# Kernel tuning notes

Hardware: AMD Instinct MI355X
Metric: run time of the kernel (lower is better)

## Reference

```python
import jax, jax.numpy as jnp
import numpy as np

B, S, D, H, DC, HC, M = 2, 2048, 1024, 16, 64, 16, 4096
DH = D // H  # head_dim = 64


def _ln(x, g, b, eps=1e-5):
    m = jnp.mean(x, axis=-1, keepdims=True)
    v = jnp.var(x, axis=-1, keepdims=True)
    return (x - m) * jax.lax.rsqrt(v + eps) * g + b


def setup_inputs() -> dict:
    key = jax.random.key(0)
    ks = jax.random.split(key, 10)
    def w(k, shape, fan_in):
        return jax.random.normal(k, shape, jnp.float32) * (fan_in ** -0.5)
    return {
        "h": jax.random.normal(ks[0], (B, S, D), jnp.float32),
        "z": jax.random.normal(ks[1], (B, S, DC), jnp.float32),
        # Linear weights stored [in, out] (transpose of torch layout)
        "wv": w(ks[2], (D, D), D),   "bv": jnp.zeros((D,), jnp.float32),
        "wca": w(ks[3], (DC, H * HC), DC), "bca": jnp.zeros((H * HC,), jnp.float32),
        "wcn": w(ks[4], (D, DC), D), "bcn": jnp.zeros((DC,), jnp.float32),
        "wo": w(ks[5], (D, D), D),   "bo": jnp.zeros((D,), jnp.float32),
        "gamma": jnp.zeros((1, H, 1, 1), jnp.float32),
        "w1": w(ks[6], (D, M), D),   "b1": jnp.zeros((M,), jnp.float32),
        "w2": w(ks[7], (M, D), M),   "b2": jnp.zeros((D,), jnp.float32),
        "ln1_g": jnp.ones((D,), jnp.float32),  "ln1_b": jnp.zeros((D,), jnp.float32),
        "ln2_g": jnp.ones((D,), jnp.float32),  "ln2_b": jnp.zeros((D,), jnp.float32),
        "lnc_g": jnp.ones((DC,), jnp.float32), "lnc_b": jnp.zeros((DC,), jnp.float32),
    }


def reference(h, z, wv, bv, wca, bca, wcn, bcn, wo, bo, gamma,
              w1, b1, w2, b2, ln1_g, ln1_b, ln2_g, ln2_b, lnc_g, lnc_b):
    hn = _ln(h, ln1_g, ln1_b)
    # values: [B,S,H,DH]
    value = (hn @ wv + bv).reshape(B, S, H, DH)
    # per-head coordinates: [B,S,H,HC]
    zh = (z @ wca + bca).reshape(B, S, H, HC)
    # pairwise squared distances per head: ||zq||^2 + ||zk||^2 - 2 zq.zk
    z_sq = jnp.sum(zh * zh, axis=-1).transpose(0, 2, 1)        # [B,H,S]
    dot = jnp.einsum('bqhc,bkhc->bhqk', zh, zh)                # [B,H,S,S]
    sq_dist = jnp.maximum(z_sq[:, :, :, None] + z_sq[:, :, None, :] - 2.0 * dot, 0.0)
    g = jax.nn.softplus(gamma)                                 # [1,H,1,1]
    attn = jax.nn.softmax(-g * sq_dist, axis=-1)               # [B,H,S,S]
    attn_out = jnp.einsum('bhqk,bkhd->bqhd', attn, value).reshape(B, S, D)
    h_attn = attn_out @ wo + bo
    z_next = hn @ wcn + bcn
    h = h + h_attn
    # FFN (dropout is identity in eval); torch GELU default is exact (erf)
    hn2 = _ln(h, ln2_g, ln2_b)
    ffn = jax.nn.gelu(hn2 @ w1 + b1, approximate=False) @ w2 + b2
    h = h + ffn
    z_out = _ln(z + z_next, lnc_g, lnc_b)
    return h, z_out
```

## Files before the change

### kernel.cpp

```cpp
#include <hip/hip_runtime.h>

#define USH unsigned short

__device__ __forceinline__ float b2f(USH u) {
    union { unsigned int i; float f; } x; x.i = ((unsigned int)u) << 16; return x.f;
}
__device__ __forceinline__ USH f2b(float f) {
    union { float f; unsigned int i; } x; x.f = f;
    unsigned int r = x.i + (0x7fffu + ((x.i >> 16) & 1u));
    return (USH)(r >> 16);
}
__device__ __forceinline__ float ldf(const USH* p)  { return b2f(*p); }
__device__ __forceinline__ float ldf(const float* p){ return *p; }
__device__ __forceinline__ void stf(USH* p, float v)  { *p = f2b(v); }
__device__ __forceinline__ void stf(float* p, float v){ *p = v; }

#define GLOAD16(gp, lp) __builtin_amdgcn_global_load_lds(                     \
    (const __attribute__((address_space(1))) void*)(gp),                      \
    (__attribute__((address_space(3))) void*)(lp), 16, 0, 0)

typedef __attribute__((ext_vector_type(8))) __bf16 bf16x8;
typedef __attribute__((ext_vector_type(4))) float  floatx4;

__global__ __launch_bounds__(256) void transpose_f2b(const float* __restrict__ W,
                                                     USH* __restrict__ WT,
                                                     int K, int N) {
    __shared__ USH t[64][72];
    int n0 = blockIdx.x * 64, k0 = blockIdx.y * 64;
    int tid = threadIdx.x;
    int kr = tid >> 4, nc = (tid & 15) * 4;
#pragma unroll
    for (int r = 0; r < 4; r++) {
        int k = kr + r * 16;
        float4 v = *(const float4*)(W + (size_t)(k0 + k) * N + n0 + nc);
        t[nc + 0][k] = f2b(v.x); t[nc + 1][k] = f2b(v.y);
        t[nc + 2][k] = f2b(v.z); t[nc + 3][k] = f2b(v.w);
    }
    __syncthreads();
    int nr = tid >> 2, kc = (tid & 3) * 8;
#pragma unroll
    for (int r = 0; r < 2; r++) {
        int k = kc + r * 32;
        *(int4*)(WT + (size_t)(n0 + nr) * K + k0 + k) = *(const int4*)&t[nr][k];
    }
}

template <typename TX>
__global__ __launch_bounds__(256) void ln_rows(const TX* __restrict__ x,
                                               const float* __restrict__ g,
                                               const float* __restrict__ bb,
                                               USH* __restrict__ y) {
    int row = blockIdx.x, tid = threadIdx.x;
    const TX* xr = x + (size_t)row * 1024 + tid * 4;
    float v[4];
#pragma unroll
    for (int i = 0; i < 4; i++) v[i] = ldf(xr + i);
    float s  = v[0] + v[1] + v[2] + v[3];
    float ss = v[0]*v[0] + v[1]*v[1] + v[2]*v[2] + v[3]*v[3];
#pragma unroll
    for (int o = 32; o; o >>= 1) { s += __shfl_down(s, o); ss += __shfl_down(ss, o); }
    __shared__ float red[10];
    int w = tid >> 6;
    if ((tid & 63) == 0) { red[w] = s; red[4 + w] = ss; }
    __syncthreads();
    if (tid == 0) {
        float S = red[0] + red[1] + red[2] + red[3];
        float SS = red[4] + red[5] + red[6] + red[7];
        float mean = S * (1.f / 1024.f);
        float var  = SS * (1.f / 1024.f) - mean * mean;
        red[8] = mean; red[9] = rsqrtf(var + 1e-5f);
    }
    __syncthreads();
    float mean = red[8], rstd = red[9];
    USH* yr = y + (size_t)row * 1024 + tid * 4;
#pragma unroll
    for (int i = 0; i < 4; i++) {
        int c = tid * 4 + i;
        yr[i] = f2b((v[i] - mean) * rstd * g[c] + bb[c]);
    }
}

__global__ __launch_bounds__(256) void zh_kernel(const float* __restrict__ z,
                                                 const float* __restrict__ wca,
                                                 const float* __restrict__ bca,
                                                 const float* __restrict__ gamma,
                                                 USH* __restrict__ zq_pack,
                                                 USH* __restrict__ zk_pack) {
    int row = blockIdx.x, n = threadIdx.x;
    __shared__ float zrow[64];
    if (n < 64) zrow[n] = z[(size_t)row * 64 + n];
    __syncthreads();
    float s = bca[n];
#pragma unroll 8
    for (int k = 0; k < 64; k++) s = fmaf(zrow[k], wca[(size_t)k * 256 + n], s);
    int h = n >> 4, c = n & 15;
    float gvl = log1pf(__expf(gamma[h])) * 1.44269504f;
    USH u = f2b(s);
    float sv = b2f(u);
    float sq = sv * sv;
    sq += __shfl_xor(sq, 1); sq += __shfl_xor(sq, 2);
    sq += __shfl_xor(sq, 4); sq += __shfl_xor(sq, 8);
    size_t base = ((size_t)h * 4096 + row) * 32;
    zk_pack[base + c] = u;
    zq_pack[base + c] = f2b(2.f * gvl * s);
    if (c == 0) {
        USH hi = f2b(sq);
        float lo = sq - b2f(hi);
        unsigned int kw0 = 0x3F80u | ((unsigned int)hi << 16);
        unsigned int kw1 = (unsigned int)f2b(lo);
        uint4 kv = {kw0, kw1, 0u, 0u};
        uint4 zz = {0u, 0u, 0u, 0u};
        *(uint4*)(zk_pack + base + 16) = kv;
        *(uint4*)(zk_pack + base + 24) = zz;
        unsigned int qw0 = (unsigned int)f2b(-gvl * sq) | ((unsigned int)f2b(-gvl) << 16);
        unsigned int qw1 = (unsigned int)f2b(-gvl);
        uint4 qv = {qw0, qw1, 0u, 0u};
        *(uint4*)(zq_pack + base + 16) = qv;
        *(uint4*)(zq_pack + base + 24) = zz;
    }
}

template <int EPI, int MI, int NI, int KB, typename TRES, typename TOUT>
__global__ __launch_bounds__(256) void gemm_kernel(const USH* __restrict__ A,
                                                   const USH* __restrict__ WT,
                                                   const float* __restrict__ bias,
                                                   const TRES* __restrict__ res,
                                                   TOUT* __restrict__ out,
                                                   int M, int N, int K) {
    constexpr int BM  = MI * 32;
    constexpr int BN  = NI * 32;
    constexpr int GR  = KB / 8;
    constexpr int RPC = 2048 / KB;
    constexpr int ACH = BM / RPC;
    constexpr int BCH = BN / RPC;
    __shared__ __align__(16) USH lA[BM][KB];
    __shared__ __align__(16) USH lB[BN][KB];
    int tid = threadIdx.x;
    int lane = tid & 63, wave = tid >> 6;
    int wr = wave >> 1, wc = wave & 1;
    int quad = lane >> 4, l15 = lane & 15;
    int m0 = blockIdx.x * BM, n0 = blockIdx.y * BN;

    int srow = tid / GR;
    int kg   = tid % GR;
    int scol = (kg ^ (srow & 7)) * 8;

    const USH* gA = A + (size_t)(m0 + srow) * K + scol;
    const USH* gB = WT + (size_t)(n0 + srow) * K + scol;
    USH* lA0 = &lA[0][0] + tid * 8;
    USH* lB0 = &lB[0][0] + tid * 8;
    int xo = (l15 & 7) * 8;

    floatx4 acc[MI][NI] = {};

    for (int k0 = 0; k0 < K; k0 += KB) {
#pragma unroll
        for (int c = 0; c < ACH; c++)
            GLOAD16(gA + (size_t)c * RPC * K + k0, lA0 + c * 2048);
#pragma unroll
        for (int c = 0; c < BCH; c++)
            GLOAD16(gB + (size_t)c * RPC * K + k0, lB0 + c * 2048);
        __syncthreads();

#pragma unroll
        for (int ks = 0; ks < KB / 32; ks++) {
            bf16x8 bfr[NI];
#pragma unroll
            for (int ni = 0; ni < NI; ni++)
                bfr[ni] = *(const bf16x8*)&lB[wc * (NI * 16) + ni * 16 + l15][(ks * 32 + quad * 8) ^ xo];
#pragma unroll
            for (int mi = 0; mi < MI; mi++) {
                bf16x8 afr = *(const bf16x8*)&lA[wr * (MI * 16) + mi * 16 + l15][(ks * 32 + quad * 8) ^ xo];
#pragma unroll
                for (int ni = 0; ni < NI; ni++)
                    acc[mi][ni] = __builtin_amdgcn_mfma_f32_16x16x32_bf16(afr, bfr[ni], acc[mi][ni], 0, 0, 0);
            }
        }
        __syncthreads();
    }

    float bias_v[NI];
#pragma unroll
    for (int ni = 0; ni < NI; ni++) bias_v[ni] = bias[n0 + wc * (NI * 16) + ni * 16 + l15];

#pragma unroll
    for (int mi = 0; mi < MI; mi++) {
#pragma unroll
        for (int r = 0; r < 4; r++) {
            int row = m0 + wr * (MI * 16) + mi * 16 + quad * 4 + r;
            size_t base = (size_t)row * N;
#pragma unroll
            for (int ni = 0; ni < NI; ni++) {
                int col = n0 + wc * (NI * 16) + ni * 16 + l15;
                float v = acc[mi][ni][r] + bias_v[ni];
                if (EPI == 2) {
                    float t = v * v;
                    float a = fmaf(t, -0.0713548162726f, -1.59576912161f);
                    v = v * __builtin_amdgcn_rcpf(1.f + __expf(v * a));
                }
                if (EPI == 1 || EPI == 3) v += ldf(res + base + col);
                stf(out + base + col, v);
            }
        }
    }
}

__global__ __launch_bounds__(512) void attn13_kernel(const USH* __restrict__ zq_pack,
                                                     const USH* __restrict__ zk_pack,
                                                     const USH* __restrict__ value,
                                                     USH* __restrict__ attn_out) {
    int b = blockIdx.x >> 4, h = blockIdx.x & 15;
    int q0 = blockIdx.y * 128;
    int tid = threadIdx.x, lane = tid & 63, wq = tid >> 6;
    int quad = lane >> 4, l15 = lane & 15;

    __shared__ __align__(16) USH KbT[2][64][40];
    __shared__ __align__(16) USH VbT[2][64][72];

    const size_t zrow0 = (size_t)b * 2048;
    const USH* zq = zq_pack + ((size_t)h * 4096 + zrow0) * 32;
    const USH* zk = zk_pack + ((size_t)h * 4096 + zrow0) * 32;
    const size_t vbase = zrow0 * 1024 + h * 64;

    bf16x8 afragQ = *(const bf16x8*)(zq + (size_t)(q0 + wq * 16 + l15) * 32 + quad * 8);

    union { unsigned int u[4]; bf16x8 v; } onesu;
#pragma unroll
    for (int i = 0; i < 4; i++) onesu.u[i] = 0x3F803F80u;
    bf16x8 ones = onesu.v;

    floatx4 oacc[4] = {};
    floatx4 lacc = {};

    int kp   = tid & 31;
    int key2 = kp * 2;
    int dh0  = (tid >> 5) * 8;
    int lg   = key2 >> 5, ll = key2 & 31;
    int cb   = lg * 32 + ((ll >> 2) & 3) * 8 + ((ll >> 4) & 1) * 4 + (ll & 3);
    int krow = (tid - 256) >> 2, kc0 = ((tid - 256) & 3) * 8;
    int4 vta, vtb; uint4 kreg;

    if (tid < 256) {
        const USH* s0 = value + vbase + (size_t)key2 * 1024 + dh0;
        vta = *(const int4*)s0;
        vtb = *(const int4*)(s0 + 1024);
        const USH* ua = (const USH*)&vta;
        const USH* ub = (const USH*)&vtb;
#pragma unroll
        for (int e = 0; e < 8; e++) {
            unsigned int dw = (unsigned int)ua[e] | ((unsigned int)ub[e] << 16);
            *(unsigned int*)&VbT[0][dh0 + e][cb] = dw;
        }
        const USH* s1 = value + vbase + (size_t)(64 + key2) * 1024 + dh0;
        vta = *(const int4*)s1;
        vtb = *(const int4*)(s1 + 1024);
    } else {
        kreg = *(const uint4*)(zk + (size_t)krow * 32 + kc0);
        *(uint4*)&KbT[0][krow][kc0] = kreg;
        kreg = *(const uint4*)(zk + (size_t)(64 + krow) * 32 + kc0);
    }

    for (int it = 0; it < 32; it++) {
        int cur = it & 1;
        __syncthreads();
        if (it + 1 < 32) {
            if (tid < 256) {
                const USH* ua = (const USH*)&vta;
                const USH* ub = (const USH*)&vtb;
#pragma unroll
                for (int e = 0; e < 8; e++) {
                    unsigned int dw = (unsigned int)ua[e] | ((unsigned int)ub[e] << 16);
                    *(unsigned int*)&VbT[cur ^ 1][dh0 + e][cb] = dw;
                }
                if (it + 2 < 32) {
                    const USH* s0 = value + vbase + (size_t)((it + 2) * 64 + key2) * 1024 + dh0;
                    vta = *(const int4*)s0;
                    vtb = *(const int4*)(s0 + 1024);
                }
            } else {
                *(uint4*)&KbT[cur ^ 1][krow][kc0] = kreg;
                if (it + 2 < 32)
                    kreg = *(const uint4*)(zk + (size_t)((it + 2) * 64 + krow) * 32 + kc0);
            }
        }

        floatx4 sacc[4];
#pragma unroll
        for (int ni = 0; ni < 4; ni++) {
            bf16x8 bkn = *(const bf16x8*)&KbT[cur][ni * 16 + l15][quad * 8];
            floatx4 zz = {};
            sacc[ni] = __builtin_amdgcn_mfma_f32_16x16x32_bf16(bkn, afragQ, zz, 0, 0, 0);
        }

        bf16x8 ap[2];
#pragma unroll
        for (int ks2 = 0; ks2 < 2; ks2++) {
            union { unsigned int u[4]; bf16x8 v; } pu;
#pragma unroll
            for (int d = 0; d < 4; d++) {
                int hi = d >> 1;
                union { float f; unsigned int i; } a, c;
                a.f = exp2f(sacc[2 * ks2 + hi][(d & 1) * 2 + 0]);
                c.f = exp2f(sacc[2 * ks2 + hi][(d & 1) * 2 + 1]);
                pu.u[d] = (a.i >> 16) | (c.i & 0xFFFF0000u);
            }
            ap[ks2] = pu.v;
        }

#pragma unroll
        for (int ks2 = 0; ks2 < 2; ks2++) {
            bf16x8 bv[4];
#pragma unroll
            for (int nd = 0; nd < 4; nd++)
                bv[nd] = *(const bf16x8*)&VbT[cur][nd * 16 + l15][ks2 * 32 + quad * 8];
#pragma unroll
            for (int nd = 0; nd < 4; nd++)
                oacc[nd] = __builtin_amdgcn_mfma_f32_16x16x32_bf16(ap[ks2], bv[nd], oacc[nd], 0, 0, 0);
            lacc = __builtin_amdgcn_mfma_f32_16x16x32_bf16(ap[ks2], ones, lacc, 0, 0, 0);
        }
    }

#pragma unroll
    for (int r = 0; r < 4; r++) {
        float inv = 1.f / lacc[r];
        int row = q0 + wq * 16 + quad * 4 + r;
        USH* o = attn_out + (zrow0 + row) * 1024 + h * 64;
#pragma unroll
        for (int nd = 0; nd < 4; nd++) o[nd * 16 + l15] = f2b(oacc[nd][r] * inv);
    }
}

__global__ __launch_bounds__(64) void lnc_kernel(const float* __restrict__ z,
                                                 const float* __restrict__ zn,
                                                 const float* __restrict__ g,
                                                 const float* __restrict__ bb,
                                                 float* __restrict__ out) {
    int row = blockIdx.x, t = threadIdx.x;
    float v = z[(size_t)row * 64 + t] + zn[(size_t)row * 64 + t];
    float s = v, ss = v * v;
#pragma unroll
    for (int o = 32; o; o >>= 1) { s += __shfl_xor(s, o); ss += __shfl_xor(ss, o); }
    float mean = s * (1.f / 64.f);
    float rstd = rsqrtf(ss * (1.f / 64.f) - mean * mean + 1e-5f);
    out[(size_t)row * 64 + t] = (v - mean) * rstd * g[t] + bb[t];
}

extern "C" void kernel_launch(void* const* d_in, const int* in_sizes, int n_in,
                              void* d_out, int out_size, void* d_ws, size_t ws_size,
                              hipStream_t stream) {
    char* p = (char*)d_ws;
    USH*   value   = (USH*)(p);
    USH*   attn_o  = (USH*)(p + ((size_t)8  << 20));
    USH*   wcnT    = (USH*)(p + ((size_t)8  << 20));
    USH*   zq_pack = (USH*)(p + ((size_t)16 << 20));
    USH*   zk_pack = (USH*)(p + ((size_t)20 << 20));
    USH*   hn      = (USH*)(p + ((size_t)24 << 20));
    USH*   mid     = (USH*)(p);
    USH*   hn2     = (USH*)(p + ((size_t)32 << 20));
    float* znext   = (float*)(p + ((size_t)40 << 20));
    USH*   wvT     = (USH*)(p + ((size_t)41 << 20));
    USH*   woT     = (USH*)(p + ((size_t)43 << 20));
    USH*   w1T     = (USH*)(p + ((size_t)45 << 20));
    USH*   w2T     = (USH*)(p + ((size_t)53 << 20));

    const float *h    = (const float*)d_in[0],  *z    = (const float*)d_in[1];
    const float *wv   = (const float*)d_in[2],  *bv   = (const float*)d_in[3];
    const float *wca  = (const float*)d_in[4],  *bca  = (const float*)d_in[5];
    const float *wcn  = (const float*)d_in[6],  *bcn  = (const float*)d_in[7];
    const float *wo   = (const float*)d_in[8],  *bo   = (const float*)d_in[9];
    const float *gam  = (const float*)d_in[10];
    const float *w1   = (const float*)d_in[11], *b1   = (const float*)d_in[12];
    const float *w2   = (const float*)d_in[13], *b2   = (const float*)d_in[14];
    const float *ln1g = (const float*)d_in[15], *ln1b = (const float*)d_in[16];
    const float *ln2g = (const float*)d_in[17], *ln2b = (const float*)d_in[18];
    const float *lncg = (const float*)d_in[19], *lncb = (const float*)d_in[20];

    float* out_h = (float*)d_out;
    float* out_z = out_h + (size_t)4096 * 1024;
    float* h1    = out_h;

    transpose_f2b<<<dim3(16, 16), 256, 0, stream>>>(wv, wvT, 1024, 1024);
    transpose_f2b<<<dim3(16, 16), 256, 0, stream>>>(wo, woT, 1024, 1024);
    transpose_f2b<<<dim3(64, 16), 256, 0, stream>>>(w1, w1T, 1024, 4096);
    transpose_f2b<<<dim3(16, 64), 256, 0, stream>>>(w2, w2T, 4096, 1024);
    transpose_f2b<<<dim3(1, 16),  256, 0, stream>>>(wcn, wcnT, 1024, 64);

    ln_rows<float><<<4096, 256, 0, stream>>>(h, ln1g, ln1b, hn);
    zh_kernel<<<4096, 256, 0, stream>>>(z, wca, bca, gam, zq_pack, zk_pack);
    gemm_kernel<0, 4, 2, 128, USH, USH><<<dim3(32, 16), 256, 0, stream>>>(hn, wvT, bv, (const USH*)nullptr, value, 4096, 1024, 1024);
    gemm_kernel<0, 1, 1, 64, float, float><<<dim3(128, 2), 256, 0, stream>>>(hn, wcnT, bcn, (const float*)nullptr, znext, 4096, 64, 1024);
    attn13_kernel<<<dim3(32, 16), 512, 0, stream>>>(zq_pack, zk_pack, value, attn_o);
    gemm_kernel<1, 4, 2, 128, float, float><<<dim3(32, 16), 256, 0, stream>>>(attn_o, woT, bo, h, h1, 4096, 1024, 1024);
    ln_rows<float><<<4096, 256, 0, stream>>>(h1, ln2g, ln2b, hn2);
    gemm_kernel<2, 4, 4, 64, USH, USH><<<dim3(32, 32), 256, 0, stream>>>(hn2, w1T, b1, (const USH*)nullptr, mid, 4096, 4096, 1024);
    gemm_kernel<3, 4, 2, 128, float, float><<<dim3(32, 16), 256, 0, stream>>>(mid, w2T, b2, h1, out_h, 4096, 1024, 4096);
    lnc_kernel<<<4096, 64, 0, stream>>>(z, znext, lncg, lncb, out_z);
}
```

Baseline: 355.7 us.

## Switch attention to 32x32 MFMA tiles with key-split waves and LDS merge

Rewrites the attention kernel to use 32x32x16 bf16 MFMA instructions instead of 16x16x32. Each block's 8 waves now form 4 query groups of 32 rows times 2 key halves. The two key halves are reduced through a shared-memory merge at the end. The V transpose staging is rebuilt with a new load/pack pattern, and launch bounds request 4 blocks per CU. The goal is fewer MFMA and LDS-read instructions per tile. In exchange it adds an end-of-kernel reduction with several barriers and uses more accumulator registers.

```diff
diff --git a/kernel.cpp b/kernel.cpp
--- a/kernel.cpp
+++ b/kernel.cpp
@@ -19,8 +19,9 @@
     (const __attribute__((address_space(1))) void*)(gp),                      \
     (__attribute__((address_space(3))) void*)(lp), 16, 0, 0)
 
-typedef __attribute__((ext_vector_type(8))) __bf16 bf16x8;
-typedef __attribute__((ext_vector_type(4))) float  floatx4;
+typedef __attribute__((ext_vector_type(8)))  __bf16 bf16x8;
+typedef __attribute__((ext_vector_type(4)))  float  floatx4;
+typedef __attribute__((ext_vector_type(16))) float  floatx16;
 
 __global__ __launch_bounds__(256) void transpose_f2b(const float* __restrict__ W,
                                                      USH* __restrict__ WT,
@@ -205,55 +206,73 @@
     }
 }
 
-__global__ __launch_bounds__(512) void attn13_kernel(const USH* __restrict__ zq_pack,
-                                                     const USH* __restrict__ zk_pack,
-                                                     const USH* __restrict__ value,
-                                                     USH* __restrict__ attn_out) {
+__global__ __launch_bounds__(512, 4) void attn16_kernel(const USH* __restrict__ zq_pack,
+                                                        const USH* __restrict__ zk_pack,
+                                                        const USH* __restrict__ value,
+                                                        USH* __restrict__ attn_out) {
     int b = blockIdx.x >> 4, h = blockIdx.x & 15;
     int q0 = blockIdx.y * 128;
     int tid = threadIdx.x, lane = tid & 63, wq = tid >> 6;
-    int quad = lane >> 4, l15 = lane & 15;
-
-    __shared__ __align__(16) USH KbT[2][64][40];
-    __shared__ __align__(16) USH VbT[2][64][72];
+    int qc = wq & 3, kg = wq >> 2;
+    int l31 = lane & 31, lh = lane >> 5;
+
+    __shared__ __align__(16) char smem[28672];
+    typedef USH KbT_t[64][40];
+    typedef USH VbT_t[64][72];
+    KbT_t* KbT = reinterpret_cast<KbT_t*>(smem);
+    VbT_t* VbT = reinterpret_cast<VbT_t*>(smem + 10240);
+    float (*mrg)[64][20] = reinterpret_cast<float(*)[64][20]>(smem);
 
     const size_t zrow0 = (size_t)b * 2048;
     const USH* zq = zq_pack + ((size_t)h * 4096 + zrow0) * 32;
     const USH* zk = zk_pack + ((size_t)h * 4096 + zrow0) * 32;
     const size_t vbase = zrow0 * 1024 + h * 64;
 
-    bf16x8 afragQ = *(const bf16x8*)(zq + (size_t)(q0 + wq * 16 + l15) * 32 + quad * 8);
+    bf16x8 qf0 = *(const bf16x8*)(zq + (size_t)(q0 + qc * 32 + l31) * 32 + lh * 8);
+    bf16x8 qf1 = *(const bf16x8*)(zq + (size_t)(q0 + qc * 32 + l31) * 32 + 16 + lh * 8);
 
     union { unsigned int u[4]; bf16x8 v; } onesu;
 #pragma unroll
     for (int i = 0; i < 4; i++) onesu.u[i] = 0x3F803F80u;
     bf16x8 ones = onesu.v;
 
-    floatx4 oacc[4] = {};
-    floatx4 lacc = {};
-
-    int kp   = tid & 31;
-    int key2 = kp * 2;
-    int dh0  = (tid >> 5) * 8;
-    int lg   = key2 >> 5, ll = key2 & 31;
-    int cb   = lg * 32 + ((ll >> 2) & 3) * 8 + ((ll >> 4) & 1) * 4 + (ll & 3);
+    floatx16 oacc0 = {}, oacc1 = {}, lacc = {};
+
+    int kp   = tid >> 4;
+    int dhc  = tid & 15;
+    int key0 = kp * 4;
+    int cb   = (kp >> 3) * 32 + ((kp >> 2) & 1) * 16 + (kp & 1) * 8 + ((kp >> 1) & 1) * 4;
     int krow = (tid - 256) >> 2, kc0 = ((tid - 256) & 3) * 8;
-    int4 vta, vtb; uint4 kreg;
+    unsigned int vlo[4], vhi[4]; uint4 kreg;
+
+#define VLOAD(ktv) do {                                                        \
+        const USH* s_ = value + vbase + (size_t)((ktv) + key0) * 1024 + dhc * 2; \
+        _Pragma("unroll")                                                      \
+        for (int i_ = 0; i_ < 4; i_++) {                                       \
+            vlo[i_] = *(const unsigned int*)(s_ + (size_t)i_ * 1024);          \
+            vhi[i_] = *(const unsigned int*)(s_ + (size_t)i_ * 1024 + 32);     \
+        } } while (0)
+
+#define VWRITE(bufv) do {                                                      \
+        uint2 w_;                                                              \
+        w_.x = (vlo[0] & 0xFFFFu) | (vlo[1] << 16);                            \
+        w_.y = (vlo[2] & 0xFFFFu) | (vlo[3] << 16);                            \
+        *(uint2*)&VbT[bufv][2 * dhc][cb] = w_;                                 \
+        w_.x = (vlo[0] >> 16) | (vlo[1] & 0xFFFF0000u);                        \
+        w_.y = (vlo[2] >> 16) | (vlo[3] & 0xFFFF0000u);                        \
+        *(uint2*)&VbT[bufv][2 * dhc + 1][cb] = w_;                             \
+        w_.x = (vhi[0] & 0xFFFFu) | (vhi[1] << 16);                            \
+        w_.y = (vhi[2] & 0xFFFFu) | (vhi[3] << 16);                            \
+        *(uint2*)&VbT[bufv][2 * dhc + 32][cb] = w_;                            \
+        w_.x = (vhi[0] >> 16) | (vhi[1] & 0xFFFF0000u);                        \
+        w_.y = (vhi[2] >> 16) | (vhi[3] & 0xFFFF0000u);                        \
+        *(uint2*)&VbT[bufv][2 * dhc + 33][cb] = w_;                            \
+    } while (0)
 
     if (tid < 256) {
-        const USH* s0 = value + vbase + (size_t)key2 * 1024 + dh0;
-        vta = *(const int4*)s0;
-        vtb = *(const int4*)(s0 + 1024);
-        const USH* ua = (const USH*)&vta;
-        const USH* ub = (const USH*)&vtb;
-#pragma unroll
-        for (int e = 0; e < 8; e++) {
-            unsigned int dw = (unsigned int)ua[e] | ((unsigned int)ub[e] << 16);
-            *(unsigned int*)&VbT[0][dh0 + e][cb] = dw;
-        }
-        const USH* s1 = value + vbase + (size_t)(64 + key2) * 1024 + dh0;
-        vta = *(const int4*)s1;
-        vtb = *(const int4*)(s1 + 1024);
+        VLOAD(0);
+        VWRITE(0);
+        VLOAD(64);
     } else {
         kreg = *(const uint4*)(zk + (size_t)krow * 32 + kc0);
         *(uint4*)&KbT[0][krow][kc0] = kreg;
@@ -265,18 +284,8 @@
         __syncthreads();
         if (it + 1 < 32) {
             if (tid < 256) {
-                const USH* ua = (const USH*)&vta;
-                const USH* ub = (const USH*)&vtb;
-#pragma unroll
-                for (int e = 0; e < 8; e++) {
-                    unsigned int dw = (unsigned int)ua[e] | ((unsigned int)ub[e] << 16);
-                    *(unsigned int*)&VbT[cur ^ 1][dh0 + e][cb] = dw;
-                }
-                if (it + 2 < 32) {
-                    const USH* s0 = value + vbase + (size_t)((it + 2) * 64 + key2) * 1024 + dh0;
-                    vta = *(const int4*)s0;
-                    vtb = *(const int4*)(s0 + 1024);
-                }
+                VWRITE(cur ^ 1);
+                if (it + 2 < 32) VLOAD((it + 2) * 64);
             } else {
                 *(uint4*)&KbT[cur ^ 1][krow][kc0] = kreg;
                 if (it + 2 < 32)
@@ -284,49 +293,74 @@
             }
         }
 
-        floatx4 sacc[4];
-#pragma unroll
-        for (int ni = 0; ni < 4; ni++) {
-            bf16x8 bkn = *(const bf16x8*)&KbT[cur][ni * 16 + l15][quad * 8];
-            floatx4 zz = {};
-            sacc[ni] = __builtin_amdgcn_mfma_f32_16x16x32_bf16(bkn, afragQ, zz, 0, 0, 0);
-        }
+        bf16x8 kf0 = *(const bf16x8*)&KbT[cur][kg * 32 + l31][lh * 8];
+        bf16x8 kf1 = *(const bf16x8*)&KbT[cur][kg * 32 + l31][16 + lh * 8];
+        floatx16 zz = {};
+        floatx16 sacc = __builtin_amdgcn_mfma_f32_32x32x16_bf16(kf0, qf0, zz, 0, 0, 0);
+        sacc = __builtin_amdgcn_mfma_f32_32x32x16_bf16(kf1, qf1, sacc, 0, 0, 0);
 
         bf16x8 ap[2];
 #pragma unroll
-        for (int ks2 = 0; ks2 < 2; ks2++) {
+        for (int m = 0; m < 2; m++) {
             union { unsigned int u[4]; bf16x8 v; } pu;
 #pragma unroll
             for (int d = 0; d < 4; d++) {
-                int hi = d >> 1;
                 union { float f; unsigned int i; } a, c;
-                a.f = exp2f(sacc[2 * ks2 + hi][(d & 1) * 2 + 0]);
-                c.f = exp2f(sacc[2 * ks2 + hi][(d & 1) * 2 + 1]);
+                a.f = exp2f(sacc[m * 8 + 2 * d + 0]);
+                c.f = exp2f(sacc[m * 8 + 2 * d + 1]);
                 pu.u[d] = (a.i >> 16) | (c.i & 0xFFFF0000u);
             }
-            ap[ks2] = pu.v;
-        }
-
-#pragma unroll
-        for (int ks2 = 0; ks2 < 2; ks2++) {
-            bf16x8 bv[4];
-#pragma unroll
-            for (int nd = 0; nd < 4; nd++)
-                bv[nd] = *(const bf16x8*)&VbT[cur][nd * 16 + l15][ks2 * 32 + quad * 8];
-#pragma unroll
-            for (int nd = 0; nd < 4; nd++)
-                oacc[nd] = __builtin_amdgcn_mfma_f32_16x16x32_bf16(ap[ks2], bv[nd], oacc[nd], 0, 0, 0);
-            lacc = __builtin_amdgcn_mfma_f32_16x16x32_bf16(ap[ks2], ones, lacc, 0, 0, 0);
-        }
-    }
-
-#pragma unroll
-    for (int r = 0; r < 4; r++) {
-        float inv = 1.f / lacc[r];
-        int row = q0 + wq * 16 + quad * 4 + r;
-        USH* o = attn_out + (zrow0 + row) * 1024 + h * 64;
-#pragma unroll
-        for (int nd = 0; nd < 4; nd++) o[nd * 16 + l15] = f2b(oacc[nd][r] * inv);
+            ap[m] = pu.v;
+        }
+
+#pragma unroll
+        for (int m = 0; m < 2; m++) {
+            bf16x8 bv0 = *(const bf16x8*)&VbT[cur][l31][kg * 32 + m * 16 + lh * 8];
+            bf16x8 bv1 = *(const bf16x8*)&VbT[cur][32 + l31][kg * 32 + m * 16 + lh * 8];
+            oacc0 = __builtin_amdgcn_mfma_f32_32x32x16_bf16(ap[m], bv0, oacc0, 0, 0, 0);
+            oacc1 = __builtin_amdgcn_mfma_f32_32x32x16_bf16(ap[m], bv1, oacc1, 0, 0, 0);
+            lacc  = __builtin_amdgcn_mfma_f32_32x32x16_bf16(ap[m], ones, lacc, 0, 0, 0);
+        }
+    }
+#undef VLOAD
+#undef VWRITE
+
+    __syncthreads();
+    if (kg == 1) {
+#pragma unroll
+        for (int r = 0; r < 16; r++) mrg[qc][lane][r] = oacc0[r];
+    }
+    __syncthreads();
+    if (kg == 0) {
+#pragma unroll
+        for (int r = 0; r < 16; r++) oacc0[r] += mrg[qc][lane][r];
+    }
+    __syncthreads();
+    if (kg == 1) {
+#pragma unroll
+        for (int r = 0; r < 16; r++) mrg[qc][lane][r] = oacc1[r];
+    }
+    __syncthreads();
+    if (kg == 0) {
+#pragma unroll
+        for (int r = 0; r < 16; r++) oacc1[r] += mrg[qc][lane][r];
+    }
+    __syncthreads();
+    if (kg == 1) {
+#pragma unroll
+        for (int r = 0; r < 16; r++) mrg[qc][lane][r] = lacc[r];
+    }
+    __syncthreads();
+
+    if (kg == 0) {
+#pragma unroll
+        for (int r = 0; r < 16; r++) {
+            float inv = 1.f / (lacc[r] + mrg[qc][lane][r]);
+            int row = q0 + qc * 32 + (r & 3) + 8 * (r >> 2) + 4 * lh;
+            USH* o = attn_out + (zrow0 + row) * 1024 + h * 64 + l31;
+            o[0]  = f2b(oacc0[r] * inv);
+            o[32] = f2b(oacc1[r] * inv);
+        }
     }
 }
 
@@ -389,7 +423,7 @@
     zh_kernel<<<4096, 256, 0, stream>>>(z, wca, bca, gam, zq_pack, zk_pack);
     gemm_kernel<0, 4, 2, 128, USH, USH><<<dim3(32, 16), 256, 0, stream>>>(hn, wvT, bv, (const USH*)nullptr, value, 4096, 1024, 1024);
     gemm_kernel<0, 1, 1, 64, float, float><<<dim3(128, 2), 256, 0, stream>>>(hn, wcnT, bcn, (const float*)nullptr, znext, 4096, 64, 1024);
-    attn13_kernel<<<dim3(32, 16), 512, 0, stream>>>(zq_pack, zk_pack, value, attn_o);
+    attn16_kernel<<<dim3(32, 16), 512, 0, stream>>>(zq_pack, zk_pack, value, attn_o);
     gemm_kernel<1, 4, 2, 128, float, float><<<dim3(32, 16), 256, 0, stream>>>(attn_o, woT, bo, h, h1, 4096, 1024, 1024);
     ln_rows<float><<<4096, 256, 0, stream>>>(h1, ln2g, ln2b, hn2);
     gemm_kernel<2, 4, 4, 64, USH, USH><<<dim3(32, 32), 256, 0, stream>>>(hn2, w1T, b1, (const USH*)nullptr, mid, 4096, 4096, 1024);
```

Result: slower. 365.6 us (+2.8%).
